# Kernel tuning notes

Hardware: AMD Instinct MI355X
Metric: run time of the kernel (lower is better)

The kernel has to match this reference:

```python
import jax, jax.numpy as jnp
import numpy as np

B, D, NCLS = 65536, 784, 10

def sparse_layer(x, idx, w, b):
    # x: [B, D]; idx: [Dout, k] int; w: [Dout, k]; b: [Dout]
    # out[b, n] = sum_j x[b, idx[n, j]] * w[n, j] + b[n]
    g = x[:, idx]                      # [B, Dout, k] gather
    return jnp.einsum('bnk,nk->bn', g, w) + b

def setup_inputs() -> dict:
    key = jax.random.key(0)
    ks = jax.random.split(key, 12)
    def rn(k, shape, scale):
        return jax.random.normal(k, shape, dtype=jnp.float32) * scale
    return {
        'x': rn(ks[0], (B, D), 1.0),
        'idx1': jax.random.randint(ks[1], (D, 2), 0, D, dtype=jnp.int32),
        'w1': rn(ks[2], (D, 2), 0.5),
        'b1': rn(ks[3], (D,), 0.1),
        'idx2': jax.random.randint(ks[4], (D, 4), 0, D, dtype=jnp.int32),
        'w2': rn(ks[5], (D, 4), 0.4),
        'b2': rn(ks[6], (D,), 0.1),
        'idx3': jax.random.randint(ks[7], (D, 8), 0, D, dtype=jnp.int32),
        'w3': rn(ks[8], (D, 8), 0.3),
        'b3': rn(ks[9], (D,), 0.1),
        'fc_w': rn(ks[10], (NCLS, D), 0.05),
        'fc_b': rn(ks[11], (NCLS,), 0.05),
    }

def reference(x, idx1, w1, b1, idx2, w2, b2, idx3, w3, b3, fc_w, fc_b):
    h = jax.nn.gelu(sparse_layer(x, idx1, w1, b1), approximate=False)
    h = jax.nn.gelu(sparse_layer(h, idx2, w2, b2), approximate=False)
    h = jax.nn.gelu(sparse_layer(h, idx3, w3, b3), approximate=False)
    logits = h @ fc_w.T + fc_b          # [B, 10]
    return jax.nn.softmax(logits, axis=-1)
```

## Files before the change

### kernel.cpp

```cpp
#include <hip/hip_runtime.h>

#define D_    784
#define ROWS  8
#define NCLS  10
#define BLOCK 512
#define NB    (65536 / ROWS)
#define NPG   4

__device__ __forceinline__ float gelu_f(float x) {
    float x2    = x * x;
    float inner = fmaf(0.044715f * x, x2, x);
    float e     = exp2f(2.3022082f * inner);
    float r     = __builtin_amdgcn_rcpf(e + 1.0f);
    return fmaf(-x, r, x);
}

__device__ __forceinline__ void fma4(float4& a, const float4& h4, float wk) {
    a.x = fmaf(h4.x, wk, a.x);
    a.y = fmaf(h4.y, wk, a.y);
    a.z = fmaf(h4.z, wk, a.z);
    a.w = fmaf(h4.w, wk, a.w);
}

template <int K>
__device__ __forceinline__ void loadIdxW(const int* __restrict__ idx,
                                         const float* __restrict__ w,
                                         int n, int* jc, float* wc) {
    if constexpr (K == 2) {
        int2   j = *(const int2*)(idx + n * 2);
        float2 v = *(const float2*)(w + n * 2);
        jc[0] = j.x; jc[1] = j.y; wc[0] = v.x; wc[1] = v.y;
    } else if constexpr (K == 4) {
        int4   j = *(const int4*)(idx + n * 4);
        float4 v = *(const float4*)(w + n * 4);
        jc[0] = j.x; jc[1] = j.y; jc[2] = j.z; jc[3] = j.w;
        wc[0] = v.x; wc[1] = v.y; wc[2] = v.z; wc[3] = v.w;
    } else {
        int4   ja = *(const int4*)(idx + n * 8);
        int4   jb = *(const int4*)(idx + n * 8 + 4);
        float4 va = *(const float4*)(w + n * 8);
        float4 vb = *(const float4*)(w + n * 8 + 4);
        jc[0] = ja.x; jc[1] = ja.y; jc[2] = ja.z; jc[3] = ja.w;
        jc[4] = jb.x; jc[5] = jb.y; jc[6] = jb.z; jc[7] = jb.w;
        wc[0] = va.x; wc[1] = va.y; wc[2] = va.z; wc[3] = va.w;
        wc[4] = vb.x; wc[5] = vb.y; wc[6] = vb.z; wc[7] = vb.w;
    }
}

template <int K>
__device__ __forceinline__ void layer_fn(const float* __restrict__ src,
                                         float* __restrict__ dst,
                                         const int* __restrict__ idx,
                                         const float* __restrict__ w,
                                         const float* __restrict__ bias,
                                         int g, int q) {
    int   jc[K];
    float wc[K];
    float bc;
    loadIdxW<K>(idx, w, g, jc, wc);
    bc = bias[g];
#pragma unroll 1
    for (int i = 0; i < NPG; ++i) {
        int n  = g + 256 * i;
        int nn = n + 256;
        int   jn[K]; float wn[K]; float bn = 0.f;
#pragma unroll
        for (int k = 0; k < K; ++k) { jn[k] = 0; wn[k] = 0.f; }
        if (nn < D_) {
            loadIdxW<K>(idx, w, nn, jn, wn);
            bn = bias[nn];
        }
        if (n < D_) {
            float4 a = make_float4(bc, bc, bc, bc);
#pragma unroll
            for (int k = 0; k < K; ++k) {
                float4 hv = *(const float4*)(src + jc[k] * 8 + q * 4);
                fma4(a, hv, wc[k]);
            }
            *(float4*)(dst + n * 8 + q * 4) =
                make_float4(gelu_f(a.x), gelu_f(a.y), gelu_f(a.z), gelu_f(a.w));
        }
#pragma unroll
        for (int k = 0; k < K; ++k) { jc[k] = jn[k]; wc[k] = wn[k]; }
        bc = bn;
    }
    __syncthreads();
}

__global__ __launch_bounds__(BLOCK)
void circnn_kernel(const float* __restrict__ x,
                   const int* __restrict__ idx1, const float* __restrict__ w1, const float* __restrict__ b1,
                   const int* __restrict__ idx2, const float* __restrict__ w2, const float* __restrict__ b2,
                   const int* __restrict__ idx3, const float* __restrict__ w3, const float* __restrict__ b3,
                   const float* __restrict__ fcw, const float* __restrict__ fcb,
                   float* __restrict__ out) {
    __shared__ __align__(16) float bufA[D_ * ROWS];
    __shared__ __align__(16) float bufB[D_ * ROWS];
    __shared__ float logits[ROWS * NCLS];

    const int tid  = threadIdx.x;
    const int g    = tid >> 1;
    const int q    = tid & 1;
    const int row0 = blockIdx.x * ROWS;

    const float* xb = x + (size_t)row0 * D_;
#pragma unroll
    for (int c2 = 0; c2 < 2; ++c2) {
#pragma unroll 1
        for (int n = tid; n < D_; n += BLOCK) {
            float4 v;
            v.x = xb[(c2 * 4 + 0) * D_ + n];
            v.y = xb[(c2 * 4 + 1) * D_ + n];
            v.z = xb[(c2 * 4 + 2) * D_ + n];
            v.w = xb[(c2 * 4 + 3) * D_ + n];
            *(float4*)(bufA + n * 8 + c2 * 4) = v;
        }
    }
    __syncthreads();

    layer_fn<2>(bufA, bufB, idx1, w1, b1, g, q);
    layer_fn<4>(bufB, bufA, idx2, w2, b2, g, q);
    layer_fn<8>(bufA, bufB, idx3, w3, b3, g, q);

    float4* part4 = (float4*)bufA;
    if (tid < 128) {
        const int jj = tid >> 1;
        const int qq = tid & 1;
        float4 facc[NCLS];
#pragma unroll
        for (int c = 0; c < NCLS; ++c) facc[c] = make_float4(0.f, 0.f, 0.f, 0.f);
#pragma unroll 1
        for (int i = 0; i < 13; ++i) {
            int n = jj + 64 * i;
            if (n < D_) {
                float4 hv = *(const float4*)(bufB + n * 8 + qq * 4);
#pragma unroll
                for (int c = 0; c < NCLS; ++c)
                    fma4(facc[c], hv, fcw[c * D_ + n]);
            }
        }
#pragma unroll
        for (int c = 0; c < NCLS; ++c)
            part4[(jj * 2 + qq) * NCLS + c] = facc[c];
    }
    __syncthreads();

    if (tid < ROWS * NCLS) {
        int r = tid / NCLS, c = tid - r * NCLS;
        int qq = r >> 2, comp = r & 3;
        const float* pf = (const float*)part4;
        float s = fcb[c];
#pragma unroll 4
        for (int jj = 0; jj < 64; ++jj)
            s += pf[((jj * 2 + qq) * NCLS + c) * 4 + comp];
        logits[tid] = s;
    }
    __syncthreads();

    if (tid < ROWS * NCLS) {
        int r = tid / NCLS;
        const float* lg = logits + r * NCLS;
        float m = lg[0];
#pragma unroll
        for (int c = 1; c < NCLS; ++c) m = fmaxf(m, lg[c]);
        float s = 0.f;
#pragma unroll
        for (int c = 0; c < NCLS; ++c) s += __expf(lg[c] - m);
        out[(size_t)row0 * NCLS + tid] = __expf(logits[tid] - m) / s;
    }
}

extern "C" void kernel_launch(void* const* d_in, const int* in_sizes, int n_in,
                              void* d_out, int out_size, void* d_ws, size_t ws_size,
                              hipStream_t stream) {
    const float* x    = (const float*)d_in[0];
    const int*   idx1 = (const int*)d_in[1];
    const float* w1   = (const float*)d_in[2];
    const float* b1   = (const float*)d_in[3];
    const int*   idx2 = (const int*)d_in[4];
    const float* w2   = (const float*)d_in[5];
    const float* b2   = (const float*)d_in[6];
    const int*   idx3 = (const int*)d_in[7];
    const float* w3   = (const float*)d_in[8];
    const float* b3   = (const float*)d_in[9];
    const float* fcw  = (const float*)d_in[10];
    const float* fcb  = (const float*)d_in[11];
    float* out = (float*)d_out;

    circnn_kernel<<<dim3(NB), dim3(BLOCK), 0, stream>>>(
        x, idx1, w1, b1, idx2, w2, b2, idx3, w3, b3, fcw, fcb, out);
}
```

Measured before the change: 434.0 us.

## Split row halves into planar LDS layout, one neuron per thread, parallelize FC

Changes the LDS activation layout from interleaved 8-row vectors to two planes of 4 rows each. Each of 768 threads now computes all 8 rows for one neuron, plus a tail of 16 neurons handled by the first threads. The FC partial sums are spread over 512 threads and reduced with warp shuffles. The aim is fewer redundant index/weight loads and more parallelism in the FC stage. In exchange the block size rises, the tail loop leaves most threads idle, and launch bounds now ask for 6 blocks per CU.

```diff
diff --git a/kernel.cpp b/kernel.cpp
--- a/kernel.cpp
+++ b/kernel.cpp
@@ -1,11 +1,12 @@
 #include <hip/hip_runtime.h>
 
-#define D_    784
-#define ROWS  8
-#define NCLS  10
-#define BLOCK 512
-#define NB    (65536 / ROWS)
-#define NPG   4
+#define D_     784
+#define ROWS   8
+#define NCLS   10
+#define BLOCK  768
+#define NB     (65536 / ROWS)
+#define PL     (D_ * 4)
+#define TAIL   (D_ - BLOCK)
 
 __device__ __forceinline__ float gelu_f(float x) {
     float x2    = x * x;
@@ -13,6 +14,10 @@
     float e     = exp2f(2.3022082f * inner);
     float r     = __builtin_amdgcn_rcpf(e + 1.0f);
     return fmaf(-x, r, x);
+}
+
+__device__ __forceinline__ float4 gelu4(const float4& a) {
+    return make_float4(gelu_f(a.x), gelu_f(a.y), gelu_f(a.z), gelu_f(a.w));
 }
 
 __device__ __forceinline__ void fma4(float4& a, const float4& h4, float wk) {
@@ -48,46 +53,31 @@
 }
 
 template <int K>
-__device__ __forceinline__ void layer_fn(const float* __restrict__ src,
-                                         float* __restrict__ dst,
-                                         const int* __restrict__ idx,
-                                         const float* __restrict__ w,
-                                         const float* __restrict__ bias,
-                                         int g, int q) {
+__device__ __forceinline__ void layer_one(const float* __restrict__ src,
+                                          float* __restrict__ dst,
+                                          const int* __restrict__ idx,
+                                          const float* __restrict__ w,
+                                          const float* __restrict__ bias,
+                                          int n) {
     int   jc[K];
     float wc[K];
-    float bc;
-    loadIdxW<K>(idx, w, g, jc, wc);
-    bc = bias[g];
-#pragma unroll 1
-    for (int i = 0; i < NPG; ++i) {
-        int n  = g + 256 * i;
-        int nn = n + 256;
-        int   jn[K]; float wn[K]; float bn = 0.f;
-#pragma unroll
-        for (int k = 0; k < K; ++k) { jn[k] = 0; wn[k] = 0.f; }
-        if (nn < D_) {
-            loadIdxW<K>(idx, w, nn, jn, wn);
-            bn = bias[nn];
-        }
-        if (n < D_) {
-            float4 a = make_float4(bc, bc, bc, bc);
-#pragma unroll
-            for (int k = 0; k < K; ++k) {
-                float4 hv = *(const float4*)(src + jc[k] * 8 + q * 4);
-                fma4(a, hv, wc[k]);
-            }
-            *(float4*)(dst + n * 8 + q * 4) =
-                make_float4(gelu_f(a.x), gelu_f(a.y), gelu_f(a.z), gelu_f(a.w));
-        }
-#pragma unroll
-        for (int k = 0; k < K; ++k) { jc[k] = jn[k]; wc[k] = wn[k]; }
-        bc = bn;
-    }
-    __syncthreads();
-}
-
-__global__ __launch_bounds__(BLOCK)
+    loadIdxW<K>(idx, w, n, jc, wc);
+    float  bc = bias[n];
+    float4 lo = make_float4(bc, bc, bc, bc);
+    float4 hi = lo;
+#pragma unroll
+    for (int k = 0; k < K; ++k) {
+        const float* g = src + jc[k] * 4;
+        float4 gl = *(const float4*)g;
+        float4 gh = *(const float4*)(g + PL);
+        fma4(lo, gl, wc[k]);
+        fma4(hi, gh, wc[k]);
+    }
+    *(float4*)(dst + n * 4)      = gelu4(lo);
+    *(float4*)(dst + n * 4 + PL) = gelu4(hi);
+}
+
+__global__ __launch_bounds__(BLOCK, 6)
 void circnn_kernel(const float* __restrict__ x,
                    const int* __restrict__ idx1, const float* __restrict__ w1, const float* __restrict__ b1,
                    const int* __restrict__ idx2, const float* __restrict__ w2, const float* __restrict__ b2,
@@ -99,49 +89,72 @@
     __shared__ float logits[ROWS * NCLS];
 
     const int tid  = threadIdx.x;
-    const int g    = tid >> 1;
-    const int q    = tid & 1;
     const int row0 = blockIdx.x * ROWS;
 
     const float* xb = x + (size_t)row0 * D_;
-#pragma unroll
-    for (int c2 = 0; c2 < 2; ++c2) {
-#pragma unroll 1
-        for (int n = tid; n < D_; n += BLOCK) {
-            float4 v;
-            v.x = xb[(c2 * 4 + 0) * D_ + n];
-            v.y = xb[(c2 * 4 + 1) * D_ + n];
-            v.z = xb[(c2 * 4 + 2) * D_ + n];
-            v.w = xb[(c2 * 4 + 3) * D_ + n];
-            *(float4*)(bufA + n * 8 + c2 * 4) = v;
-        }
-    }
-    __syncthreads();
-
-    layer_fn<2>(bufA, bufB, idx1, w1, b1, g, q);
-    layer_fn<4>(bufB, bufA, idx2, w2, b2, g, q);
-    layer_fn<8>(bufA, bufB, idx3, w3, b3, g, q);
+    {
+        int n = tid;
+        float4 lo, hi;
+        lo.x = xb[0 * D_ + n]; lo.y = xb[1 * D_ + n];
+        lo.z = xb[2 * D_ + n]; lo.w = xb[3 * D_ + n];
+        hi.x = xb[4 * D_ + n]; hi.y = xb[5 * D_ + n];
+        hi.z = xb[6 * D_ + n]; hi.w = xb[7 * D_ + n];
+        *(float4*)(bufA + n * 4)      = lo;
+        *(float4*)(bufA + n * 4 + PL) = hi;
+    }
+    if (tid < TAIL) {
+        int n = BLOCK + tid;
+        float4 lo, hi;
+        lo.x = xb[0 * D_ + n]; lo.y = xb[1 * D_ + n];
+        lo.z = xb[2 * D_ + n]; lo.w = xb[3 * D_ + n];
+        hi.x = xb[4 * D_ + n]; hi.y = xb[5 * D_ + n];
+        hi.z = xb[6 * D_ + n]; hi.w = xb[7 * D_ + n];
+        *(float4*)(bufA + n * 4)      = lo;
+        *(float4*)(bufA + n * 4 + PL) = hi;
+    }
+    __syncthreads();
+
+    layer_one<2>(bufA, bufB, idx1, w1, b1, tid);
+    if (tid < TAIL) layer_one<2>(bufA, bufB, idx1, w1, b1, BLOCK + tid);
+    __syncthreads();
+
+    layer_one<4>(bufB, bufA, idx2, w2, b2, tid);
+    if (tid < TAIL) layer_one<4>(bufB, bufA, idx2, w2, b2, BLOCK + tid);
+    __syncthreads();
+
+    layer_one<8>(bufA, bufB, idx3, w3, b3, tid);
+    if (tid < TAIL) layer_one<8>(bufA, bufB, idx3, w3, b3, BLOCK + tid);
+    __syncthreads();
 
     float4* part4 = (float4*)bufA;
-    if (tid < 128) {
-        const int jj = tid >> 1;
-        const int qq = tid & 1;
+    if (tid < 512) {
+        const int p  = tid & 3;
+        const int qq = (tid >> 2) & 1;
+        const int jj = tid >> 3;
         float4 facc[NCLS];
 #pragma unroll
         for (int c = 0; c < NCLS; ++c) facc[c] = make_float4(0.f, 0.f, 0.f, 0.f);
 #pragma unroll 1
-        for (int i = 0; i < 13; ++i) {
-            int n = jj + 64 * i;
+        for (int i = p; i < 13; i += 4) {
+            int n = jj + (i << 6);
             if (n < D_) {
-                float4 hv = *(const float4*)(bufB + n * 8 + qq * 4);
+                float4 hv = *(const float4*)(bufB + qq * PL + n * 4);
 #pragma unroll
                 for (int c = 0; c < NCLS; ++c)
                     fma4(facc[c], hv, fcw[c * D_ + n]);
             }
         }
-#pragma unroll
-        for (int c = 0; c < NCLS; ++c)
-            part4[(jj * 2 + qq) * NCLS + c] = facc[c];
+        float* f = (float*)facc;
+#pragma unroll
+        for (int t = 0; t < 4 * NCLS; ++t) {
+            f[t] += __shfl_xor(f[t], 1);
+            f[t] += __shfl_xor(f[t], 2);
+        }
+        if (p == 0) {
+#pragma unroll
+            for (int c = 0; c < NCLS; ++c)
+                part4[(jj * 2 + qq) * NCLS + c] = facc[c];
+        }
     }
     __syncthreads();
 
```

After: 492.6 us. 13.5% more time.
